# Optimization experiments

Hardware: AMD Instinct MI355X
Metric: run time of the kernel (lower is better)

Reference implementation:

```python
import jax, jax.numpy as jnp
import numpy as np

N = 50000   # nodes
E = 800000  # edges (avg degree 16)
IN = 3      # in_feats = value(1) + u(2)
H = 128     # hid_feats


def setup_inputs() -> dict:
    key = jax.random.key(0)
    ks = jax.random.split(key, 24)
    value = jax.random.normal(ks[0], (N, 1), jnp.float32)
    u = jax.random.normal(ks[1], (N, 2), jnp.float32)
    src = jax.random.randint(ks[2], (E,), 0, N, dtype=jnp.int32)
    dst = jax.random.randint(ks[3], (E,), 0, N, dtype=jnp.int32)
    dims = [IN, H // 2, H, H, H, H, H, H, H, H, 1]
    inp = {"value": value, "u": u, "src": src, "dst": dst}
    for i in range(10):
        inp[f"W{i+1}"] = jax.random.normal(ks[4 + i], (dims[i], dims[i + 1]), jnp.float32) / np.sqrt(dims[i]).astype(np.float32)
        inp[f"b{i+1}"] = jnp.zeros((dims[i + 1],), jnp.float32)
    return inp


def _gconv(x, src, dst, inv_deg, W, b):
    # DGL GraphConv norm='right': sum incoming src features, divide by in-degree, linear, bias
    agg = jax.ops.segment_sum(x[src], dst, num_segments=N)  # [N, d_in]
    return (agg * inv_deg) @ W + b


def reference(value, u, src, dst, W1, b1, W2, b2, W3, b3, W4, b4, W5, b5,
              W6, b6, W7, b7, W8, b8, W9, b9, W10, b10):
    deg = jax.ops.segment_sum(jnp.ones((E,), jnp.float32), dst, num_segments=N)
    inv_deg = (1.0 / jnp.clip(deg, 1.0))[:, None]  # DGL clamps in-degree to >=1
    lrelu = lambda h: jax.nn.leaky_relu(h, 0.01)
    x = jnp.concatenate([value, u], axis=1)  # [N, 3]
    h = _gconv(x, src, dst, inv_deg, W1, b1)
    h = lrelu(_gconv(h, src, dst, inv_deg, W2, b2))
    h = lrelu(_gconv(h, src, dst, inv_deg, W3, b3))
    h = lrelu(_gconv(h, src, dst, inv_deg, W4, b4))
    h = _gconv(h, src, dst, inv_deg, W5, b5)
    h = _gconv(h, src, dst, inv_deg, W6, b6)
    h = _gconv(h, src, dst, inv_deg, W7, b7)
    h = _gconv(h, src, dst, inv_deg, W8, b8)
    h = jax.nn.sigmoid(_gconv(h, src, dst, inv_deg, W9, b9))
    h = _gconv(h, src, dst, inv_deg, W10, b10)  # [N, 1]
    return h
```

## Files before the change

### kernel.cpp

```cpp
#include <hip/hip_runtime.h>
#include <math.h>

typedef unsigned int u32;
typedef unsigned short u16;
using bf16x8 = __attribute__((ext_vector_type(8))) short;
using f32x4 = __attribute__((ext_vector_type(4))) float;

__device__ inline float bf_lo(u32 v) { return __uint_as_float(v << 16); }
__device__ inline float bf_hi(u32 v) { return __uint_as_float(v & 0xFFFF0000u); }
__device__ inline u16 f2bf(float f) {
    u32 u = __float_as_uint(f);
    return (u16)((u + 0x7FFFu + ((u >> 16) & 1u)) >> 16);
}
__device__ inline float bf2f(u16 h) { return __uint_as_float((u32)h << 16); }
__device__ inline float invdeg(int d) { return 1.0f / (float)(d > 1 ? d : 1); }

#define BIN_SHIFT 13

struct W7 { const float* p[7]; };

__global__ __launch_bounds__(256) void k_front(const int* __restrict__ src,
                                               const int* __restrict__ dst,
                                               int* __restrict__ cur,
                                               u16* __restrict__ colp,
                                               int E, int EB, int SB,
                                               const float* __restrict__ value,
                                               const float* __restrict__ u,
                                               float4* __restrict__ x4, int n, int NBx4,
                                               W7 wp, const float* __restrict__ W64,
                                               u16* __restrict__ hi128, u16* __restrict__ lo128,
                                               u16* __restrict__ hi64, u16* __restrict__ lo64) {
    int blk = blockIdx.x;
    if (blk < SB) {
        const int bin = blk / EB;
        int e = (blk - bin * EB) * 256 + threadIdx.x;
        if (e >= E) return;
        int d = dst[e];
        if ((d >> BIN_SHIFT) != bin) return;
        int slot = atomicAdd(&cur[d], 1);
        if (slot < 64) colp[(size_t)d * 64 + slot] = (u16)src[e];
        return;
    }
    int pb = blk - SB;
    if (pb < NBx4) {
        int i = pb * 256 + threadIdx.x;
        if (i < n) x4[i] = make_float4(value[i], u[2 * i], u[2 * i + 1], 0.f);
        return;
    }
    pb -= NBx4;
    if (pb < 56) {
        const int l = pb >> 3;
        const float* W = wp.p[l];
        int g = (pb & 7) * 256 + threadIdx.x;
        int ct = g >> 8;
        int rem = g & 255;
        int ks = rem >> 6;
        int lane = rem & 63;
        int kbase = ks * 32 + ((lane >> 4) << 3);
        int nn = (ct << 4) + (lane & 15);
        size_t off = ((size_t)l * 2048 + g) * 8;
#pragma unroll
        for (int j = 0; j < 8; ++j) {
            float w = W[(size_t)(kbase + j) * 128 + nn];
            u16 h = f2bf(w);
            hi128[off + j] = h;
            lo128[off + j] = f2bf(w - bf2f(h));
        }
    } else {
        int g = (pb - 56) * 256 + threadIdx.x;
        int ct = g >> 7;
        int rem = g & 127;
        int ks = rem >> 6;
        int lane = rem & 63;
        int kbase = ks * 32 + ((lane >> 4) << 3);
        int nn = (ct << 4) + (lane & 15);
        size_t off = (size_t)g * 8;
#pragma unroll
        for (int j = 0; j < 8; ++j) {
            float w = W64[(size_t)(kbase + j) * 128 + nn];
            u16 h = f2bf(w);
            hi64[off + j] = h;
            lo64[off + j] = f2bf(w - bf2f(h));
        }
    }
}

__global__ __launch_bounds__(256) void k_l1(const float4* __restrict__ x4,
                                            const u16* __restrict__ colp,
                                            const int* __restrict__ deg,
                                            const float* __restrict__ W1,
                                            const float* __restrict__ b1,
                                            u16* __restrict__ out, int nNodes) {
    const int lane = threadIdx.x & 63;
    const int n = blockIdx.x * 4 + (threadIdx.x >> 6);
    if (n >= nNodes) return;
    int dfull = deg[n];
    int dg = dfull > 64 ? 64 : dfull;
    const u16* cl = colp + (size_t)n * 64;
    float a0 = 0.f, a1 = 0.f, a2 = 0.f;
    if (lane < dg) {
        float4 v = x4[cl[lane]];
        a0 = v.x; a1 = v.y; a2 = v.z;
    }
#pragma unroll
    for (int o = 32; o; o >>= 1) {
        a0 += __shfl_xor(a0, o, 64);
        a1 += __shfl_xor(a1, o, 64);
        a2 += __shfl_xor(a2, o, 64);
    }
    float iv = invdeg(dfull);
    float y = b1[lane] + iv * (a0 * W1[lane] + a1 * W1[64 + lane] + a2 * W1[128 + lane]);
    out[(size_t)n * 64 + lane] = f2bf(y);
}

template <int DIN>
__global__ __launch_bounds__(256) void k_aggq(const uint4* __restrict__ H4,
                                              const u16* __restrict__ colp,
                                              const int* __restrict__ deg,
                                              uint4* __restrict__ out, int nNodes) {
    constexpr int LPN = DIN / 8;
    constexpr int NPW = 64 / LPN;
    const int tid = threadIdx.x;
    const int lane = tid & 63;
    const int wv = tid >> 6;
    const int g = lane / LPN;
    const int c = lane % LPN;
    const int n = (blockIdx.x * 4 + wv) * NPW + g;
    const int nn = n < nNodes ? n : nNodes - 1;
    const int dfull = deg[nn];
    const int dg = dfull > 64 ? 64 : dfull;
    const u16* cl = colp + (size_t)nn * 64;

    int dgm = dg;
#pragma unroll
    for (int o = 32; o; o >>= 1) {
        int t = __shfl_xor(dgm, o, 64);
        dgm = t > dgm ? t : dgm;
    }

    float acc0 = 0.f, acc1 = 0.f, acc2 = 0.f, acc3 = 0.f;
    float acc4 = 0.f, acc5 = 0.f, acc6 = 0.f, acc7 = 0.f;

    for (int j = 0; j < dgm; j += 8) {
        uint4 iv4 = *reinterpret_cast<const uint4*>(cl + j);
        int s0 = (int)(iv4.x & 0xFFFFu), s1 = (int)(iv4.x >> 16);
        int s2 = (int)(iv4.y & 0xFFFFu), s3 = (int)(iv4.y >> 16);
        int s4 = (int)(iv4.z & 0xFFFFu), s5 = (int)(iv4.z >> 16);
        int s6 = (int)(iv4.w & 0xFFFFu), s7 = (int)(iv4.w >> 16);
        bool k0 = j + 0 < dg, k1 = j + 1 < dg, k2 = j + 2 < dg, k3 = j + 3 < dg;
        bool k4 = j + 4 < dg, k5 = j + 5 < dg, k6 = j + 6 < dg, k7 = j + 7 < dg;
        if (!k0) s0 = 0; if (!k1) s1 = 0; if (!k2) s2 = 0; if (!k3) s3 = 0;
        if (!k4) s4 = 0; if (!k5) s5 = 0; if (!k6) s6 = 0; if (!k7) s7 = 0;
        uint4 v0 = H4[(size_t)s0 * LPN + c];
        uint4 v1 = H4[(size_t)s1 * LPN + c];
        uint4 v2 = H4[(size_t)s2 * LPN + c];
        uint4 v3 = H4[(size_t)s3 * LPN + c];
        uint4 v4 = H4[(size_t)s4 * LPN + c];
        uint4 v5 = H4[(size_t)s5 * LPN + c];
        uint4 v6 = H4[(size_t)s6 * LPN + c];
        uint4 v7 = H4[(size_t)s7 * LPN + c];
        if (k0) { acc0 += bf_lo(v0.x); acc1 += bf_hi(v0.x); acc2 += bf_lo(v0.y); acc3 += bf_hi(v0.y);
                  acc4 += bf_lo(v0.z); acc5 += bf_hi(v0.z); acc6 += bf_lo(v0.w); acc7 += bf_hi(v0.w); }
        if (k1) { acc0 += bf_lo(v1.x); acc1 += bf_hi(v1.x); acc2 += bf_lo(v1.y); acc3 += bf_hi(v1.y);
                  acc4 += bf_lo(v1.z); acc5 += bf_hi(v1.z); acc6 += bf_lo(v1.w); acc7 += bf_hi(v1.w); }
        if (k2) { acc0 += bf_lo(v2.x); acc1 += bf_hi(v2.x); acc2 += bf_lo(v2.y); acc3 += bf_hi(v2.y);
                  acc4 += bf_lo(v2.z); acc5 += bf_hi(v2.z); acc6 += bf_lo(v2.w); acc7 += bf_hi(v2.w); }
        if (k3) { acc0 += bf_lo(v3.x); acc1 += bf_hi(v3.x); acc2 += bf_lo(v3.y); acc3 += bf_hi(v3.y);
                  acc4 += bf_lo(v3.z); acc5 += bf_hi(v3.z); acc6 += bf_lo(v3.w); acc7 += bf_hi(v3.w); }
        if (k4) { acc0 += bf_lo(v4.x); acc1 += bf_hi(v4.x); acc2 += bf_lo(v4.y); acc3 += bf_hi(v4.y);
                  acc4 += bf_lo(v4.z); acc5 += bf_hi(v4.z); acc6 += bf_lo(v4.w); acc7 += bf_hi(v4.w); }
        if (k5) { acc0 += bf_lo(v5.x); acc1 += bf_hi(v5.x); acc2 += bf_lo(v5.y); acc3 += bf_hi(v5.y);
                  acc4 += bf_lo(v5.z); acc5 += bf_hi(v5.z); acc6 += bf_lo(v5.w); acc7 += bf_hi(v5.w); }
        if (k6) { acc0 += bf_lo(v6.x); acc1 += bf_hi(v6.x); acc2 += bf_lo(v6.y); acc3 += bf_hi(v6.y);
                  acc4 += bf_lo(v6.z); acc5 += bf_hi(v6.z); acc6 += bf_lo(v6.w); acc7 += bf_hi(v6.w); }
        if (k7) { acc0 += bf_lo(v7.x); acc1 += bf_hi(v7.x); acc2 += bf_lo(v7.y); acc3 += bf_hi(v7.y);
                  acc4 += bf_lo(v7.z); acc5 += bf_hi(v7.z); acc6 += bf_lo(v7.w); acc7 += bf_hi(v7.w); }
    }

    float iv = invdeg(dfull);
    uint4 o;
    o.x = (u32)f2bf(acc0 * iv) | ((u32)f2bf(acc1 * iv) << 16);
    o.y = (u32)f2bf(acc2 * iv) | ((u32)f2bf(acc3 * iv) << 16);
    o.z = (u32)f2bf(acc4 * iv) | ((u32)f2bf(acc5 * iv) << 16);
    o.w = (u32)f2bf(acc6 * iv) | ((u32)f2bf(acc7 * iv) << 16);
    if (n < nNodes) out[(size_t)n * LPN + c] = o;
}

template <int ACT>
__device__ inline float actf(float x) {
    if (ACT == 1) return x > 0.f ? x : 0.01f * x;
    if (ACT == 2) return 1.f / (1.f + expf(-x));
    return x;
}

template <int DIN, int ACT>
__global__ __launch_bounds__(256) void k_mm(const u16* __restrict__ A,
                                            const u16* __restrict__ pkHi,
                                            const u16* __restrict__ pkLo,
                                            const float* __restrict__ B,
                                            u16* __restrict__ Y, int nNodes) {
    constexpr int NKS = DIN / 32;
    const int lane = threadIdx.x & 63;
    const int w = threadIdx.x >> 6;
    const int base = blockIdx.x * 64 + w * 16;
    const int m = lane & 15;
    const int kb = lane >> 4;
    int arow = base + m;
    if (arow >= nNodes) arow = nNodes - 1;

    bf16x8 aF[NKS];
#pragma unroll
    for (int ks = 0; ks < NKS; ++ks)
        aF[ks] = *reinterpret_cast<const bf16x8*>(A + (size_t)arow * DIN + ks * 32 + kb * 8);

    const bf16x8* bh = reinterpret_cast<const bf16x8*>(pkHi);
    const bf16x8* bl = reinterpret_cast<const bf16x8*>(pkLo);

#pragma unroll
    for (int ct = 0; ct < 8; ++ct) {
        f32x4 acc = {0.f, 0.f, 0.f, 0.f};
#pragma unroll
        for (int ks = 0; ks < NKS; ++ks) {
            acc = __builtin_amdgcn_mfma_f32_16x16x32_bf16(aF[ks], bh[(ct * NKS + ks) * 64 + lane], acc, 0, 0, 0);
            acc = __builtin_amdgcn_mfma_f32_16x16x32_bf16(aF[ks], bl[(ct * NKS + ks) * 64 + lane], acc, 0, 0, 0);
        }
        float bias = B[ct * 16 + m];
#pragma unroll
        for (int r = 0; r < 4; ++r) {
            int row = base + kb * 4 + r;
            if (row < nNodes)
                Y[(size_t)row * 128 + ct * 16 + m] = f2bf(actf<ACT>(acc[r] + bias));
        }
    }
}

__global__ __launch_bounds__(256) void k_mm_last(const u16* __restrict__ A,
                                                 const u16* __restrict__ pkHi,
                                                 const u16* __restrict__ pkLo,
                                                 const float* __restrict__ B,
                                                 const float* __restrict__ w10,
                                                 float* __restrict__ t, int nNodes) {
    const int lane = threadIdx.x & 63;
    const int w = threadIdx.x >> 6;
    const int base = blockIdx.x * 64 + w * 16;
    const int m = lane & 15;
    const int kb = lane >> 4;
    int arow = base + m;
    if (arow >= nNodes) arow = nNodes - 1;

    bf16x8 aF[4];
#pragma unroll
    for (int ks = 0; ks < 4; ++ks)
        aF[ks] = *reinterpret_cast<const bf16x8*>(A + (size_t)arow * 128 + ks * 32 + kb * 8);

    const bf16x8* bh = reinterpret_cast<const bf16x8*>(pkHi);
    const bf16x8* bl = reinterpret_cast<const bf16x8*>(pkLo);

    float p0 = 0.f, p1 = 0.f, p2 = 0.f, p3 = 0.f;
#pragma unroll
    for (int ct = 0; ct < 8; ++ct) {
        f32x4 acc = {0.f, 0.f, 0.f, 0.f};
#pragma unroll
        for (int ks = 0; ks < 4; ++ks) {
            acc = __builtin_amdgcn_mfma_f32_16x16x32_bf16(aF[ks], bh[(ct * 4 + ks) * 64 + lane], acc, 0, 0, 0);
            acc = __builtin_amdgcn_mfma_f32_16x16x32_bf16(aF[ks], bl[(ct * 4 + ks) * 64 + lane], acc, 0, 0, 0);
        }
        float bias = B[ct * 16 + m];
        float wv = w10[ct * 16 + m];
        p0 += wv * actf<2>(acc[0] + bias);
        p1 += wv * actf<2>(acc[1] + bias);
        p2 += wv * actf<2>(acc[2] + bias);
        p3 += wv * actf<2>(acc[3] + bias);
    }
#pragma unroll
    for (int o = 1; o < 16; o <<= 1) {
        p0 += __shfl_xor(p0, o, 64);
        p1 += __shfl_xor(p1, o, 64);
        p2 += __shfl_xor(p2, o, 64);
        p3 += __shfl_xor(p3, o, 64);
    }
    if (m == 0) {
        int r0 = base + kb * 4;
        if (r0 + 0 < nNodes) t[r0 + 0] = p0;
        if (r0 + 1 < nNodes) t[r0 + 1] = p1;
        if (r0 + 2 < nNodes) t[r0 + 2] = p2;
        if (r0 + 3 < nNodes) t[r0 + 3] = p3;
    }
}

__global__ __launch_bounds__(256) void k_aggs(const float* __restrict__ t,
                                              const u16* __restrict__ colp,
                                              const int* __restrict__ deg,
                                              const float* __restrict__ B,
                                              float* __restrict__ out, int nNodes) {
    int n = blockIdx.x * 256 + threadIdx.x;
    if (n >= nNodes) return;
    int dfull = deg[n];
    int dg = dfull > 64 ? 64 : dfull;
    const u16* cl = colp + (size_t)n * 64;
    float s = 0.f;
    for (int j = 0; j < dg; ++j) s += t[cl[j]];
    out[n] = s * invdeg(dfull) + B[0];
}

extern "C" void kernel_launch(void* const* d_in, const int* in_sizes, int n_in,
                              void* d_out, int out_size, void* d_ws, size_t ws_size,
                              hipStream_t stream) {
    const float* value = (const float*)d_in[0];
    const float* u = (const float*)d_in[1];
    const int* src = (const int*)d_in[2];
    const int* dst = (const int*)d_in[3];
    const float* W[10];
    const float* b[10];
    for (int i = 0; i < 10; ++i) {
        W[i] = (const float*)d_in[4 + 2 * i];
        b[i] = (const float*)d_in[5 + 2 * i];
    }
    const int N = in_sizes[0];
    const int E = in_sizes[2];
    float* out = (float*)d_out;

    char* p = (char*)d_ws;
    auto carve = [&](size_t bytes) {
        char* r = p;
        p += (bytes + 255) & ~(size_t)255;
        return r;
    };
    int* deg = (int*)carve((size_t)N * 4);
    u16* colp = (u16*)carve((size_t)N * 64 * 2);
    float4* x4 = (float4*)carve((size_t)N * 16);
    u16* hA = (u16*)carve((size_t)N * 128 * 2);
    u16* hB = (u16*)carve((size_t)N * 128 * 2);
    u16* agg = (u16*)carve((size_t)N * 128 * 2);
    float* t10 = (float*)carve((size_t)N * 4);
    u16* pk128hi = (u16*)carve((size_t)7 * 2048 * 8 * 2);
    u16* pk128lo = (u16*)carve((size_t)7 * 2048 * 8 * 2);
    u16* pk64hi = (u16*)carve((size_t)1024 * 8 * 2);
    u16* pk64lo = (u16*)carve((size_t)1024 * 8 * 2);

    const int nbins = (N + (1 << BIN_SHIFT) - 1) >> BIN_SHIFT;
    const int EB = (E + 255) / 256;
    const int SB = EB * nbins;
    const int NBx4 = (N + 255) / 256;

    hipMemsetAsync(deg, 0, (size_t)N * 4, stream);

    W7 wp;
    for (int i = 0; i < 7; ++i) wp.p[i] = W[2 + i];
    k_front<<<SB + NBx4 + 60, 256, 0, stream>>>(src, dst, deg, colp, E, EB, SB,
                                                value, u, x4, N, NBx4, wp, W[1],
                                                pk128hi, pk128lo, pk64hi, pk64lo);

    const int gw = (N + 3) / 4;
    const int gq128 = (N + 15) / 16;
    const int gq64 = (N + 31) / 32;
    const int gg = (N + 63) / 64;
    const int gt = (N + 255) / 256;
    const size_t PK = 2048 * 8;

    k_l1<<<gw, 256, 0, stream>>>(x4, colp, deg, W[0], b[0], hA, N);
    k_aggq<64><<<gq64, 256, 0, stream>>>((const uint4*)hA, colp, deg, (uint4*)agg, N);
    k_mm<64, 1><<<gg, 256, 0, stream>>>(agg, pk64hi, pk64lo, b[1], hB, N);
    k_aggq<128><<<gq128, 256, 0, stream>>>((const uint4*)hB, colp, deg, (uint4*)agg, N);
    k_mm<128, 1><<<gg, 256, 0, stream>>>(agg, pk128hi + 0 * PK, pk128lo + 0 * PK, b[2], hA, N);
    k_aggq<128><<<gq128, 256, 0, stream>>>((const uint4*)hA, colp, deg, (uint4*)agg, N);
    k_mm<128, 1><<<gg, 256, 0, stream>>>(agg, pk128hi + 1 * PK, pk128lo + 1 * PK, b[3], hB, N);
    k_aggq<128><<<gq128, 256, 0, stream>>>((const uint4*)hB, colp, deg, (uint4*)agg, N);
    k_mm<128, 0><<<gg, 256, 0, stream>>>(agg, pk128hi + 2 * PK, pk128lo + 2 * PK, b[4], hA, N);
    k_aggq<128><<<gq128, 256, 0, stream>>>((const uint4*)hA, colp, deg, (uint4*)agg, N);
    k_mm<128, 0><<<gg, 256, 0, stream>>>(agg, pk128hi + 3 * PK, pk128lo + 3 * PK, b[5], hB, N);
    k_aggq<128><<<gq128, 256, 0, stream>>>((const uint4*)hB, colp, deg, (uint4*)agg, N);
    k_mm<128, 0><<<gg, 256, 0, stream>>>(agg, pk128hi + 4 * PK, pk128lo + 4 * PK, b[6], hA, N);
    k_aggq<128><<<gq128, 256, 0, stream>>>((const uint4*)hA, colp, deg, (uint4*)agg, N);
    k_mm<128, 0><<<gg, 256, 0, stream>>>(agg, pk128hi + 5 * PK, pk128lo + 5 * PK, b[7], hB, N);
    k_aggq<128><<<gq128, 256, 0, stream>>>((const uint4*)hB, colp, deg, (uint4*)agg, N);
    k_mm_last<<<gg, 256, 0, stream>>>(agg, pk128hi + 6 * PK, pk128lo + 6 * PK, b[8], W[9], t10, N);
    k_aggs<<<gt, 256, 0, stream>>>(t10, colp, deg, b[9], out, N);
}
```

Baseline: 419.0 us.

## Fold linear layers into precomputed weight products and reorder aggregation before projection

Layers 5 through 8 have no activation, and aggregation with mean normalisation is linear, so the code multiplies W5·W6·W7·W8 and their biases into a single matrix on device. It then runs four consecutive aggregations followed by one matmul instead of alternating matmuls. Layers 1-2 are also folded: the 3-wide input, with a constant 1 column that carries the bias, is aggregated twice at width 4 before one projection by W1·W2. Four of the six 128-wide GEMMs and the 64-wide path are removed, at the cost of small weight-product kernels and a different rounding order with bf16 intermediates.

```diff
diff --git a/kernel.cpp b/kernel.cpp
--- a/kernel.cpp
+++ b/kernel.cpp
@@ -17,7 +17,7 @@
 
 #define BIN_SHIFT 13
 
-struct W7 { const float* p[7]; };
+struct W3p { const float* p[3]; };
 
 __global__ __launch_bounds__(256) void k_front(const int* __restrict__ src,
                                                const int* __restrict__ dst,
@@ -27,9 +27,8 @@
                                                const float* __restrict__ value,
                                                const float* __restrict__ u,
                                                float4* __restrict__ x4, int n, int NBx4,
-                                               W7 wp, const float* __restrict__ W64,
-                                               u16* __restrict__ hi128, u16* __restrict__ lo128,
-                                               u16* __restrict__ hi64, u16* __restrict__ lo64) {
+                                               W3p wp,
+                                               u16* __restrict__ hi128, u16* __restrict__ lo128) {
     int blk = blockIdx.x;
     if (blk < SB) {
         const int bin = blk / EB;
@@ -44,88 +43,189 @@
     int pb = blk - SB;
     if (pb < NBx4) {
         int i = pb * 256 + threadIdx.x;
-        if (i < n) x4[i] = make_float4(value[i], u[2 * i], u[2 * i + 1], 0.f);
+        if (i < n) x4[i] = make_float4(value[i], u[2 * i], u[2 * i + 1], 1.0f);
         return;
     }
     pb -= NBx4;
-    if (pb < 56) {
-        const int l = pb >> 3;
-        const float* W = wp.p[l];
-        int g = (pb & 7) * 256 + threadIdx.x;
-        int ct = g >> 8;
-        int rem = g & 255;
-        int ks = rem >> 6;
-        int lane = rem & 63;
-        int kbase = ks * 32 + ((lane >> 4) << 3);
-        int nn = (ct << 4) + (lane & 15);
-        size_t off = ((size_t)l * 2048 + g) * 8;
-#pragma unroll
-        for (int j = 0; j < 8; ++j) {
-            float w = W[(size_t)(kbase + j) * 128 + nn];
-            u16 h = f2bf(w);
-            hi128[off + j] = h;
-            lo128[off + j] = f2bf(w - bf2f(h));
+    const int l = pb >> 3;
+    const float* W = wp.p[l];
+    int g = (pb & 7) * 256 + threadIdx.x;
+    int ct = g >> 8;
+    int rem = g & 255;
+    int ks = rem >> 6;
+    int lane = rem & 63;
+    int kbase = ks * 32 + ((lane >> 4) << 3);
+    int nn = (ct << 4) + (lane & 15);
+    size_t off = ((size_t)l * 2048 + g) * 8;
+#pragma unroll
+    for (int j = 0; j < 8; ++j) {
+        float w = W[(size_t)(kbase + j) * 128 + nn];
+        u16 h = f2bf(w);
+        hi128[off + j] = h;
+        lo128[off + j] = f2bf(w - bf2f(h));
+    }
+}
+
+__global__ __launch_bounds__(256) void k_stageA(const float* __restrict__ W7, const float* __restrict__ W8,
+                                                const float* __restrict__ b7, const float* __restrict__ b8,
+                                                const float* __restrict__ W1, const float* __restrict__ W2,
+                                                const float* __restrict__ b1,
+                                                float* __restrict__ P1, float* __restrict__ bp1,
+                                                float* __restrict__ W12) {
+    int blk = blockIdx.x, tid = threadIdx.x;
+    if (blk < 64) {
+        int idx = blk * 256 + tid;
+        int r = idx >> 7, c = idx & 127;
+        float s0 = 0.f, s1 = 0.f, s2 = 0.f, s3 = 0.f;
+        for (int k = 0; k < 128; k += 4) {
+            s0 += W7[r * 128 + k + 0] * W8[(k + 0) * 128 + c];
+            s1 += W7[r * 128 + k + 1] * W8[(k + 1) * 128 + c];
+            s2 += W7[r * 128 + k + 2] * W8[(k + 2) * 128 + c];
+            s3 += W7[r * 128 + k + 3] * W8[(k + 3) * 128 + c];
+        }
+        P1[idx] = (s0 + s1) + (s2 + s3);
+    } else if (blk < 66) {
+        int idx = (blk - 64) * 256 + tid;
+        if (idx < 384) {
+            int r = idx >> 7, c = idx & 127;
+            float s = 0.f;
+            for (int k = 0; k < 64; ++k) s += W1[r * 64 + k] * W2[k * 128 + c];
+            W12[idx] = s;
+        }
+    } else if (blk == 66) {
+        if (tid < 128) {
+            float s = 0.f;
+            for (int k = 0; k < 64; ++k) s += b1[k] * W2[k * 128 + tid];
+            W12[384 + tid] = s;
         }
     } else {
-        int g = (pb - 56) * 256 + threadIdx.x;
-        int ct = g >> 7;
-        int rem = g & 127;
-        int ks = rem >> 6;
-        int lane = rem & 63;
-        int kbase = ks * 32 + ((lane >> 4) << 3);
-        int nn = (ct << 4) + (lane & 15);
-        size_t off = (size_t)g * 8;
-#pragma unroll
-        for (int j = 0; j < 8; ++j) {
-            float w = W64[(size_t)(kbase + j) * 128 + nn];
-            u16 h = f2bf(w);
-            hi64[off + j] = h;
-            lo64[off + j] = f2bf(w - bf2f(h));
-        }
-    }
-}
-
-__global__ __launch_bounds__(256) void k_l1(const float4* __restrict__ x4,
-                                            const u16* __restrict__ colp,
-                                            const int* __restrict__ deg,
-                                            const float* __restrict__ W1,
-                                            const float* __restrict__ b1,
-                                            u16* __restrict__ out, int nNodes) {
-    const int lane = threadIdx.x & 63;
-    const int n = blockIdx.x * 4 + (threadIdx.x >> 6);
+        if (tid < 128) {
+            float s = 0.f;
+            for (int k = 0; k < 128; ++k) s += b7[k] * W8[k * 128 + tid];
+            bp1[tid] = s + b8[tid];
+        }
+    }
+}
+
+__global__ __launch_bounds__(256) void k_stageB(const float* __restrict__ W6,
+                                                const float* __restrict__ b6,
+                                                const float* __restrict__ P1,
+                                                const float* __restrict__ bp1,
+                                                float* __restrict__ P2, float* __restrict__ bp2) {
+    int blk = blockIdx.x, tid = threadIdx.x;
+    if (blk < 64) {
+        int idx = blk * 256 + tid;
+        int r = idx >> 7, c = idx & 127;
+        float s0 = 0.f, s1 = 0.f, s2 = 0.f, s3 = 0.f;
+        for (int k = 0; k < 128; k += 4) {
+            s0 += W6[r * 128 + k + 0] * P1[(k + 0) * 128 + c];
+            s1 += W6[r * 128 + k + 1] * P1[(k + 1) * 128 + c];
+            s2 += W6[r * 128 + k + 2] * P1[(k + 2) * 128 + c];
+            s3 += W6[r * 128 + k + 3] * P1[(k + 3) * 128 + c];
+        }
+        P2[idx] = (s0 + s1) + (s2 + s3);
+    } else {
+        if (tid < 128) {
+            float s = 0.f;
+            for (int k = 0; k < 128; ++k) s += b6[k] * P1[k * 128 + tid];
+            bp2[tid] = s + bp1[tid];
+        }
+    }
+}
+
+__global__ __launch_bounds__(256) void k_stageC(const float* __restrict__ W5,
+                                                const float* __restrict__ b5,
+                                                const float* __restrict__ P2,
+                                                const float* __restrict__ bp2,
+                                                u16* __restrict__ pkhi, u16* __restrict__ pklo,
+                                                float* __restrict__ bhat) {
+    int blk = blockIdx.x, tid = threadIdx.x;
+    if (blk < 64) {
+        int idx = blk * 256 + tid;
+        int k = idx >> 7, c = idx & 127;
+        float s0 = 0.f, s1 = 0.f, s2 = 0.f, s3 = 0.f;
+        for (int m = 0; m < 128; m += 4) {
+            s0 += W5[k * 128 + m + 0] * P2[(m + 0) * 128 + c];
+            s1 += W5[k * 128 + m + 1] * P2[(m + 1) * 128 + c];
+            s2 += W5[k * 128 + m + 2] * P2[(m + 2) * 128 + c];
+            s3 += W5[k * 128 + m + 3] * P2[(m + 3) * 128 + c];
+        }
+        float val = (s0 + s1) + (s2 + s3);
+        u16 h = f2bf(val);
+        u16 l = f2bf(val - bf2f(h));
+        int lane = (((k >> 3) & 3) << 4) | (c & 15);
+        int ct = c >> 4, ks = k >> 5, j = k & 7;
+        size_t off = ((size_t)(ct * 4 + ks) * 64 + lane) * 8 + j;
+        pkhi[off] = h;
+        pklo[off] = l;
+    } else {
+        if (tid < 128) {
+            float s = 0.f;
+            for (int k = 0; k < 128; ++k) s += b5[k] * P2[k * 128 + tid];
+            bhat[tid] = s + bp2[tid];
+        }
+    }
+}
+
+__global__ __launch_bounds__(256) void k_agg4(const float4* __restrict__ X,
+                                              const u16* __restrict__ colp,
+                                              const int* __restrict__ deg,
+                                              float4* __restrict__ out, int nNodes) {
+    int n = blockIdx.x * 256 + threadIdx.x;
     if (n >= nNodes) return;
     int dfull = deg[n];
     int dg = dfull > 64 ? 64 : dfull;
     const u16* cl = colp + (size_t)n * 64;
-    float a0 = 0.f, a1 = 0.f, a2 = 0.f;
-    if (lane < dg) {
-        float4 v = x4[cl[lane]];
-        a0 = v.x; a1 = v.y; a2 = v.z;
-    }
-#pragma unroll
-    for (int o = 32; o; o >>= 1) {
-        a0 += __shfl_xor(a0, o, 64);
-        a1 += __shfl_xor(a1, o, 64);
-        a2 += __shfl_xor(a2, o, 64);
+    float a0 = 0.f, a1 = 0.f, a2 = 0.f, a3 = 0.f;
+    int j = 0;
+    for (; j + 8 <= dg; j += 8) {
+        uint4 q = *reinterpret_cast<const uint4*>(cl + j);
+        float4 v0 = X[q.x & 0xFFFFu], v1 = X[q.x >> 16];
+        float4 v2 = X[q.y & 0xFFFFu], v3 = X[q.y >> 16];
+        float4 v4 = X[q.z & 0xFFFFu], v5 = X[q.z >> 16];
+        float4 v6 = X[q.w & 0xFFFFu], v7 = X[q.w >> 16];
+        a0 += ((v0.x + v1.x) + (v2.x + v3.x)) + ((v4.x + v5.x) + (v6.x + v7.x));
+        a1 += ((v0.y + v1.y) + (v2.y + v3.y)) + ((v4.y + v5.y) + (v6.y + v7.y));
+        a2 += ((v0.z + v1.z) + (v2.z + v3.z)) + ((v4.z + v5.z) + (v6.z + v7.z));
+        a3 += ((v0.w + v1.w) + (v2.w + v3.w)) + ((v4.w + v5.w) + (v6.w + v7.w));
+    }
+    for (; j < dg; ++j) {
+        float4 v = X[cl[j]];
+        a0 += v.x; a1 += v.y; a2 += v.z; a3 += v.w;
     }
     float iv = invdeg(dfull);
-    float y = b1[lane] + iv * (a0 * W1[lane] + a1 * W1[64 + lane] + a2 * W1[128 + lane]);
-    out[(size_t)n * 64 + lane] = f2bf(y);
-}
-
-template <int DIN>
+    out[n] = make_float4(a0 * iv, a1 * iv, a2 * iv, a3 * iv);
+}
+
+template <int ACT>
+__device__ inline float actf(float x) {
+    if (ACT == 1) return x > 0.f ? x : 0.01f * x;
+    if (ACT == 2) return 1.f / (1.f + expf(-x));
+    return x;
+}
+
+__global__ __launch_bounds__(256) void k_l2(const float4* __restrict__ y2,
+                                            const float* __restrict__ W12,
+                                            const float* __restrict__ b2,
+                                            u16* __restrict__ out, int nNodes) {
+    int node = blockIdx.x * 2 + (threadIdx.x >> 7);
+    int c = threadIdx.x & 127;
+    if (node >= nNodes) return;
+    float4 y = y2[node];
+    float r = y.x * W12[c] + y.y * W12[128 + c] + y.z * W12[256 + c] + y.w * W12[384 + c] + b2[c];
+    out[(size_t)node * 128 + c] = f2bf(actf<1>(r));
+}
+
 __global__ __launch_bounds__(256) void k_aggq(const uint4* __restrict__ H4,
                                               const u16* __restrict__ colp,
                                               const int* __restrict__ deg,
                                               uint4* __restrict__ out, int nNodes) {
-    constexpr int LPN = DIN / 8;
-    constexpr int NPW = 64 / LPN;
     const int tid = threadIdx.x;
     const int lane = tid & 63;
     const int wv = tid >> 6;
-    const int g = lane / LPN;
-    const int c = lane % LPN;
-    const int n = (blockIdx.x * 4 + wv) * NPW + g;
+    const int g = lane >> 4;
+    const int c = lane & 15;
+    const int n = (blockIdx.x * 4 + wv) * 4 + g;
     const int nn = n < nNodes ? n : nNodes - 1;
     const int dfull = deg[nn];
     const int dg = dfull > 64 ? 64 : dfull;
@@ -151,14 +251,14 @@
         bool k4 = j + 4 < dg, k5 = j + 5 < dg, k6 = j + 6 < dg, k7 = j + 7 < dg;
         if (!k0) s0 = 0; if (!k1) s1 = 0; if (!k2) s2 = 0; if (!k3) s3 = 0;
         if (!k4) s4 = 0; if (!k5) s5 = 0; if (!k6) s6 = 0; if (!k7) s7 = 0;
-        uint4 v0 = H4[(size_t)s0 * LPN + c];
-        uint4 v1 = H4[(size_t)s1 * LPN + c];
-        uint4 v2 = H4[(size_t)s2 * LPN + c];
-        uint4 v3 = H4[(size_t)s3 * LPN + c];
-        uint4 v4 = H4[(size_t)s4 * LPN + c];
-        uint4 v5 = H4[(size_t)s5 * LPN + c];
-        uint4 v6 = H4[(size_t)s6 * LPN + c];
-        uint4 v7 = H4[(size_t)s7 * LPN + c];
+        uint4 v0 = H4[(size_t)s0 * 16 + c];
+        uint4 v1 = H4[(size_t)s1 * 16 + c];
+        uint4 v2 = H4[(size_t)s2 * 16 + c];
+        uint4 v3 = H4[(size_t)s3 * 16 + c];
+        uint4 v4 = H4[(size_t)s4 * 16 + c];
+        uint4 v5 = H4[(size_t)s5 * 16 + c];
+        uint4 v6 = H4[(size_t)s6 * 16 + c];
+        uint4 v7 = H4[(size_t)s7 * 16 + c];
         if (k0) { acc0 += bf_lo(v0.x); acc1 += bf_hi(v0.x); acc2 += bf_lo(v0.y); acc3 += bf_hi(v0.y);
                   acc4 += bf_lo(v0.z); acc5 += bf_hi(v0.z); acc6 += bf_lo(v0.w); acc7 += bf_hi(v0.w); }
         if (k1) { acc0 += bf_lo(v1.x); acc1 += bf_hi(v1.x); acc2 += bf_lo(v1.y); acc3 += bf_hi(v1.y);
@@ -183,23 +283,15 @@
     o.y = (u32)f2bf(acc2 * iv) | ((u32)f2bf(acc3 * iv) << 16);
     o.z = (u32)f2bf(acc4 * iv) | ((u32)f2bf(acc5 * iv) << 16);
     o.w = (u32)f2bf(acc6 * iv) | ((u32)f2bf(acc7 * iv) << 16);
-    if (n < nNodes) out[(size_t)n * LPN + c] = o;
+    if (n < nNodes) out[(size_t)n * 16 + c] = o;
 }
 
 template <int ACT>
-__device__ inline float actf(float x) {
-    if (ACT == 1) return x > 0.f ? x : 0.01f * x;
-    if (ACT == 2) return 1.f / (1.f + expf(-x));
-    return x;
-}
-
-template <int DIN, int ACT>
 __global__ __launch_bounds__(256) void k_mm(const u16* __restrict__ A,
                                             const u16* __restrict__ pkHi,
                                             const u16* __restrict__ pkLo,
                                             const float* __restrict__ B,
                                             u16* __restrict__ Y, int nNodes) {
-    constexpr int NKS = DIN / 32;
     const int lane = threadIdx.x & 63;
     const int w = threadIdx.x >> 6;
     const int base = blockIdx.x * 64 + w * 16;
@@ -208,10 +300,10 @@
     int arow = base + m;
     if (arow >= nNodes) arow = nNodes - 1;
 
-    bf16x8 aF[NKS];
-#pragma unroll
-    for (int ks = 0; ks < NKS; ++ks)
-        aF[ks] = *reinterpret_cast<const bf16x8*>(A + (size_t)arow * DIN + ks * 32 + kb * 8);
+    bf16x8 aF[4];
+#pragma unroll
+    for (int ks = 0; ks < 4; ++ks)
+        aF[ks] = *reinterpret_cast<const bf16x8*>(A + (size_t)arow * 128 + ks * 32 + kb * 8);
 
     const bf16x8* bh = reinterpret_cast<const bf16x8*>(pkHi);
     const bf16x8* bl = reinterpret_cast<const bf16x8*>(pkLo);
@@ -220,9 +312,9 @@
     for (int ct = 0; ct < 8; ++ct) {
         f32x4 acc = {0.f, 0.f, 0.f, 0.f};
 #pragma unroll
-        for (int ks = 0; ks < NKS; ++ks) {
-            acc = __builtin_amdgcn_mfma_f32_16x16x32_bf16(aF[ks], bh[(ct * NKS + ks) * 64 + lane], acc, 0, 0, 0);
-            acc = __builtin_amdgcn_mfma_f32_16x16x32_bf16(aF[ks], bl[(ct * NKS + ks) * 64 + lane], acc, 0, 0, 0);
+        for (int ks = 0; ks < 4; ++ks) {
+            acc = __builtin_amdgcn_mfma_f32_16x16x32_bf16(aF[ks], bh[(ct * 4 + ks) * 64 + lane], acc, 0, 0, 0);
+            acc = __builtin_amdgcn_mfma_f32_16x16x32_bf16(aF[ks], bl[(ct * 4 + ks) * 64 + lane], acc, 0, 0, 0);
         }
         float bias = B[ct * 16 + m];
 #pragma unroll
@@ -329,14 +421,20 @@
     int* deg = (int*)carve((size_t)N * 4);
     u16* colp = (u16*)carve((size_t)N * 64 * 2);
     float4* x4 = (float4*)carve((size_t)N * 16);
+    float4* y1 = (float4*)carve((size_t)N * 16);
+    float4* y2 = (float4*)carve((size_t)N * 16);
     u16* hA = (u16*)carve((size_t)N * 128 * 2);
     u16* hB = (u16*)carve((size_t)N * 128 * 2);
     u16* agg = (u16*)carve((size_t)N * 128 * 2);
     float* t10 = (float*)carve((size_t)N * 4);
-    u16* pk128hi = (u16*)carve((size_t)7 * 2048 * 8 * 2);
-    u16* pk128lo = (u16*)carve((size_t)7 * 2048 * 8 * 2);
-    u16* pk64hi = (u16*)carve((size_t)1024 * 8 * 2);
-    u16* pk64lo = (u16*)carve((size_t)1024 * 8 * 2);
+    u16* pkhi = (u16*)carve((size_t)4 * 2048 * 8 * 2);
+    u16* pklo = (u16*)carve((size_t)4 * 2048 * 8 * 2);
+    float* P1 = (float*)carve((size_t)128 * 128 * 4);
+    float* P2 = (float*)carve((size_t)128 * 128 * 4);
+    float* bp1 = (float*)carve(128 * 4);
+    float* bp2 = (float*)carve(128 * 4);
+    float* bhat = (float*)carve(128 * 4);
+    float* W12 = (float*)carve(512 * 4);
 
     const int nbins = (N + (1 << BIN_SHIFT) - 1) >> BIN_SHIFT;
     const int EB = (E + 255) / 256;
@@ -345,35 +443,36 @@
 
     hipMemsetAsync(deg, 0, (size_t)N * 4, stream);
 
-    W7 wp;
-    for (int i = 0; i < 7; ++i) wp.p[i] = W[2 + i];
-    k_front<<<SB + NBx4 + 60, 256, 0, stream>>>(src, dst, deg, colp, E, EB, SB,
-                                                value, u, x4, N, NBx4, wp, W[1],
-                                                pk128hi, pk128lo, pk64hi, pk64lo);
-
-    const int gw = (N + 3) / 4;
-    const int gq128 = (N + 15) / 16;
-    const int gq64 = (N + 31) / 32;
+    W3p wp;
+    wp.p[0] = W[2];
+    wp.p[1] = W[3];
+    wp.p[2] = W[8];
+    k_front<<<SB + NBx4 + 24, 256, 0, stream>>>(src, dst, deg, colp, E, EB, SB,
+                                                value, u, x4, N, NBx4, wp, pkhi, pklo);
+    k_stageA<<<68, 256, 0, stream>>>(W[6], W[7], b[6], b[7], W[0], W[1], b[0], P1, bp1, W12);
+    k_stageB<<<65, 256, 0, stream>>>(W[5], b[5], P1, bp1, P2, bp2);
+    const size_t PK = 2048 * 8;
+    k_stageC<<<65, 256, 0, stream>>>(W[4], b[4], P2, bp2, pkhi + 3 * PK, pklo + 3 * PK, bhat);
+
+    const int ga4 = (N + 255) / 256;
+    const int gl2 = (N + 1) / 2;
+    const int gq = (N + 15) / 16;
     const int gg = (N + 63) / 64;
     const int gt = (N + 255) / 256;
-    const size_t PK = 2048 * 8;
-
-    k_l1<<<gw, 256, 0, stream>>>(x4, colp, deg, W[0], b[0], hA, N);
-    k_aggq<64><<<gq64, 256, 0, stream>>>((const uint4*)hA, colp, deg, (uint4*)agg, N);
-    k_mm<64, 1><<<gg, 256, 0, stream>>>(agg, pk64hi, pk64lo, b[1], hB, N);
-    k_aggq<128><<<gq128, 256, 0, stream>>>((const uint4*)hB, colp, deg, (uint4*)agg, N);
-    k_mm<128, 1><<<gg, 256, 0, stream>>>(agg, pk128hi + 0 * PK, pk128lo + 0 * PK, b[2], hA, N);
-    k_aggq<128><<<gq128, 256, 0, stream>>>((const uint4*)hA, colp, deg, (uint4*)agg, N);
-    k_mm<128, 1><<<gg, 256, 0, stream>>>(agg, pk128hi + 1 * PK, pk128lo + 1 * PK, b[3], hB, N);
-    k_aggq<128><<<gq128, 256, 0, stream>>>((const uint4*)hB, colp, deg, (uint4*)agg, N);
-    k_mm<128, 0><<<gg, 256, 0, stream>>>(agg, pk128hi + 2 * PK, pk128lo + 2 * PK, b[4], hA, N);
-    k_aggq<128><<<gq128, 256, 0, stream>>>((const uint4*)hA, colp, deg, (uint4*)agg, N);
-    k_mm<128, 0><<<gg, 256, 0, stream>>>(agg, pk128hi + 3 * PK, pk128lo + 3 * PK, b[5], hB, N);
-    k_aggq<128><<<gq128, 256, 0, stream>>>((const uint4*)hB, colp, deg, (uint4*)agg, N);
-    k_mm<128, 0><<<gg, 256, 0, stream>>>(agg, pk128hi + 4 * PK, pk128lo + 4 * PK, b[6], hA, N);
-    k_aggq<128><<<gq128, 256, 0, stream>>>((const uint4*)hA, colp, deg, (uint4*)agg, N);
-    k_mm<128, 0><<<gg, 256, 0, stream>>>(agg, pk128hi + 5 * PK, pk128lo + 5 * PK, b[7], hB, N);
-    k_aggq<128><<<gq128, 256, 0, stream>>>((const uint4*)hB, colp, deg, (uint4*)agg, N);
-    k_mm_last<<<gg, 256, 0, stream>>>(agg, pk128hi + 6 * PK, pk128lo + 6 * PK, b[8], W[9], t10, N);
+
+    k_agg4<<<ga4, 256, 0, stream>>>(x4, colp, deg, y1, N);
+    k_agg4<<<ga4, 256, 0, stream>>>(y1, colp, deg, y2, N);
+    k_l2<<<gl2, 256, 0, stream>>>(y2, W12, b[1], hA, N);
+    k_aggq<<<gq, 256, 0, stream>>>((const uint4*)hA, colp, deg, (uint4*)agg, N);
+    k_mm<1><<<gg, 256, 0, stream>>>(agg, pkhi + 0 * PK, pklo + 0 * PK, b[2], hB, N);
+    k_aggq<<<gq, 256, 0, stream>>>((const uint4*)hB, colp, deg, (uint4*)agg, N);
+    k_mm<1><<<gg, 256, 0, stream>>>(agg, pkhi + 1 * PK, pklo + 1 * PK, b[3], hA, N);
+    k_aggq<<<gq, 256, 0, stream>>>((const uint4*)hA, colp, deg, (uint4*)hB, N);
+    k_aggq<<<gq, 256, 0, stream>>>((const uint4*)hB, colp, deg, (uint4*)hA, N);
+    k_aggq<<<gq, 256, 0, stream>>>((const uint4*)hA, colp, deg, (uint4*)hB, N);
+    k_aggq<<<gq, 256, 0, stream>>>((const uint4*)hB, colp, deg, (uint4*)agg, N);
+    k_mm<0><<<gg, 256, 0, stream>>>(agg, pkhi + 3 * PK, pklo + 3 * PK, bhat, hA, N);
+    k_aggq<<<gq, 256, 0, stream>>>((const uint4*)hA, colp, deg, (uint4*)agg, N);
+    k_mm_last<<<gg, 256, 0, stream>>>(agg, pkhi + 2 * PK, pklo + 2 * PK, b[8], W[9], t10, N);
     k_aggs<<<gt, 256, 0, stream>>>(t10, colp, deg, b[9], out, N);
 }
```

After: 366.5 us, median of 2. 1.14x faster.
